# Performance work log

Measured on AMD Instinct MI355X. Metric: run time of the kernel, lower is better.

## Reference

```python
import jax, jax.numpy as jnp
import numpy as np

B, S, D, H = 4, 2048, 1024, 16
DK = D // H


def setup_inputs() -> dict:
    key = jax.random.key(0)
    ks = jax.random.split(key, 5)
    scale = 1.0 / np.sqrt(D)
    return {
        "embeddings": jax.random.normal(ks[0], (B, S, D), dtype=jnp.float32),
        "W_q": jax.random.normal(ks[1], (D, D), dtype=jnp.float32) * scale,
        "W_k": jax.random.normal(ks[2], (D, D), dtype=jnp.float32) * scale,
        "W_v": jax.random.normal(ks[3], (D, D), dtype=jnp.float32) * scale,
        "W_o": jax.random.normal(ks[4], (D, D), dtype=jnp.float32) * scale,
    }


def reference(embeddings, W_q, W_k, W_v, W_o):
    # torch Linear: y = x @ W.T  (weights stored [out, in])
    def proj(x, W):
        # [B,S,D] -> [B,H,S,DK]
        y = jnp.einsum("bsd,ed->bse", x, W)
        return y.reshape(B, S, H, DK).transpose(0, 2, 1, 3)

    Q = proj(embeddings, W_q)
    K = proj(embeddings, W_k)
    V = proj(embeddings, W_v)

    scores = jnp.einsum("bhqd,bhkd->bhqk", Q, K) / jnp.sqrt(jnp.float32(DK))
    p_attn = jax.nn.softmax(scores, axis=-1)  # dropout p=0.0 -> identity
    x = jnp.einsum("bhqk,bhkd->bhqd", p_attn, V)
    x = x.transpose(0, 2, 1, 3).reshape(B, S, D)
    return jnp.einsum("bsd,ed->bse", x, W_o)
```

## Files before the change

### kernel.cpp

```cpp
#include <hip/hip_runtime.h>
#include <hip/hip_bf16.h>

#define BB 4
#define SS 2048
#define DD 1024
#define HH 16
#define MM (BB * SS)

typedef __attribute__((ext_vector_type(8))) short bf16x8;
typedef __attribute__((ext_vector_type(4))) float f32x4;

__device__ __forceinline__ unsigned short f2bf(float f) {
  union { float f; unsigned u; } v; v.f = f;
  unsigned r = v.u + 0x7fffu + ((v.u >> 16) & 1u);
  return (unsigned short)(r >> 16);
}

__device__ __forceinline__ void gl2lds16(const void* g, void* l) {
  __builtin_amdgcn_global_load_lds(
      (const __attribute__((address_space(1))) unsigned int*)g,
      (__attribute__((address_space(3))) unsigned int*)l, 16, 0, 0);
}

__global__ __launch_bounds__(256)
void convall(const float* __restrict__ X, const float* __restrict__ a,
             const float* __restrict__ b, const float* __restrict__ c,
             const float* __restrict__ d, unsigned short* __restrict__ wall,
             unsigned short* __restrict__ xb) {
  int y = blockIdx.y;
  const float* s; unsigned short* o;
  if (y < 4) {
    const float* srcs[4] = {a, b, c, d};
    s = srcs[y]; o = wall + (size_t)y * 1048576;
  } else {
    s = X + (size_t)(y - 4) * 1048576; o = xb + (size_t)(y - 4) * 1048576;
  }
  int i = (blockIdx.x * 256 + threadIdx.x) * 4;
  float4 v = *(const float4*)(s + i);
  ushort4 h4; h4.x = f2bf(v.x); h4.y = f2bf(v.y); h4.z = f2bf(v.z); h4.w = f2bf(v.w);
  *(ushort4*)(o + i) = h4;
}

template<int OMODE>
__global__ __launch_bounds__(256)
void gemm_k(const unsigned short* __restrict__ A16, const unsigned short* __restrict__ Bp,
            void* __restrict__ C0p, void* __restrict__ C1p, void* __restrict__ C2p) {
  __shared__ unsigned short As[32 * 136];
  __shared__ unsigned short Bs[128 * 32];
  const int m0 = blockIdx.x * 128, n0g = blockIdx.y * 128;
  const int tid = threadIdx.x, lane = tid & 63, wave = tid >> 6;
  const int wm = (wave & 1) * 64, wn = (wave >> 1) * 64;
  const int row_in = lane & 15, quad = lane >> 4;

  f32x4 acc[4][4] = {};

  for (int kb = 0; kb < DD; kb += 32) {
    {
      int r = wave * 32 + (lane >> 2);
      const unsigned short* g = Bp + (size_t)(n0g + r) * DD + kb + (lane & 3) * 8;
      gl2lds16(g, Bs + (wave * 32) * 32);
      gl2lds16(g + (size_t)16 * DD, Bs + (wave * 32 + 16) * 32);
      const unsigned short* ga = A16 + (size_t)(m0 + r) * DD + kb + (lane & 3) * 8;
      gl2lds16(ga, As + (wave * 32) * 32);
      gl2lds16(ga + (size_t)16 * DD, As + (wave * 32 + 16) * 32);
    }
    __syncthreads();
    bf16x8 af[4], bfr[4];
#pragma unroll
    for (int i = 0; i < 4; ++i)
      af[i] = *(const bf16x8*)(As + (wm + i * 16 + row_in) * 32 + quad * 8);
#pragma unroll
    for (int j = 0; j < 4; ++j)
      bfr[j] = *(const bf16x8*)(Bs + (wn + j * 16 + row_in) * 32 + quad * 8);
#pragma unroll
    for (int i = 0; i < 4; ++i)
#pragma unroll
      for (int j = 0; j < 4; ++j)
        acc[i][j] = __builtin_amdgcn_mfma_f32_16x16x32_bf16(af[i], bfr[j], acc[i][j], 0, 0, 0);
    __syncthreads();
  }

  if (OMODE == 1) {
    float* Cout = (float*)C0p;
#pragma unroll
    for (int i = 0; i < 4; ++i)
#pragma unroll
      for (int j = 0; j < 4; ++j)
#pragma unroll
        for (int r = 0; r < 4; ++r)
          Cout[(size_t)(m0 + wm + i * 16 + quad * 4 + r) * DD + n0g + wn + j * 16 + row_in] =
              acc[i][j][r];
  } else {
    const int seg = n0g >> 10;
    if (seg < 2) {
      unsigned short* Cout = (unsigned short*)(seg == 0 ? C0p : C1p);
      const int n0 = n0g & 1023;
#pragma unroll
      for (int i = 0; i < 4; ++i)
#pragma unroll
        for (int j = 0; j < 4; ++j)
#pragma unroll
          for (int r = 0; r < 4; ++r)
            Cout[(size_t)(m0 + wm + i * 16 + quad * 4 + r) * DD + n0 + wn + j * 16 + row_in] =
                f2bf(acc[i][j][r]);
    } else {
      unsigned short* Vt = (unsigned short*)C2p;
      unsigned short* Ts = As;
      const int b = m0 >> 11, m_in_b = m0 & 2047;
      const int nv = n0g - 2048;
#pragma unroll
      for (int cn = 0; cn < 4; ++cn) {
        if ((wave >> 1) == (cn >> 1)) {
#pragma unroll
          for (int i = 0; i < 4; ++i)
#pragma unroll
            for (int jj = 0; jj < 2; ++jj)
#pragma unroll
              for (int r = 0; r < 4; ++r) {
                int j = (cn & 1) * 2 + jj;
                Ts[(jj * 16 + row_in) * 136 + wm + i * 16 + quad * 4 + r] = f2bf(acc[i][j][r]);
              }
        }
        __syncthreads();
#pragma unroll
        for (int it = 0; it < 2; ++it) {
          int cc = tid + it * 256;
          int rowL = cc >> 4, o8 = (cc & 15) * 8;
          int cbase = rowL * 136 + (o8 & 64) + ((o8 & 63) >> 2);
          ushort4 lo, hi;
          lo.x = Ts[cbase];      lo.y = Ts[cbase + 16];
          lo.z = Ts[cbase + 32]; lo.w = Ts[cbase + 48];
          hi.x = Ts[cbase + 1];  hi.y = Ts[cbase + 17];
          hi.z = Ts[cbase + 33]; hi.w = Ts[cbase + 49];
          int n = nv + cn * 32 + rowL;
          int h = n >> 6, dd = n & 63;
          unsigned short* dst = Vt + ((size_t)((b * 16 + h) * 64 + dd)) * SS + m_in_b + o8;
          *(ushort4*)dst = lo;
          *(ushort4*)(dst + 4) = hi;
        }
        __syncthreads();
      }
    }
  }
}

__global__ __launch_bounds__(256, 4)
void attn_kernel(const unsigned short* __restrict__ Q, const unsigned short* __restrict__ K,
                 const unsigned short* __restrict__ Vt_g, unsigned short* __restrict__ AO) {
  __shared__ unsigned short Ks[64 * 72];
  __shared__ unsigned short Vs[64 * 72];
  __shared__ unsigned short Ps[128 * 72];
  const int qt = blockIdx.x, bh = blockIdx.y, b = bh >> 4, h = bh & 15;
  const int tid = threadIdx.x, lane = tid & 63, w = tid >> 6;
  const int row_in = lane & 15, quad = lane >> 4;
  const float Cs = 0.180336880f;
  const float C0 = 17.3123405f;
  const size_t qbase = ((size_t)(b * SS + qt * 128)) * DD + h * 64;

  bf16x8 aq[2][2];
#pragma unroll
  for (int m = 0; m < 2; ++m) {
    const unsigned short* qp = Q + qbase + (size_t)(w * 32 + m * 16 + row_in) * DD;
    aq[m][0] = *(const bf16x8*)(qp + quad * 8);
    aq[m][1] = *(const bf16x8*)(qp + 32 + quad * 8);
  }
  f32x4 oacc[2][4] = {};
  float lrow[2][4] = {};
  const int permr = 2 * (row_in >> 2) + (row_in & 1) + 8 * ((row_in >> 1) & 1);
  const int pw_base = (w * 32) * 72;

  for (int kt = 0; kt < SS / 64; ++kt) {
    __syncthreads();
    const size_t kbase = ((size_t)(b * SS + kt * 64)) * DD + h * 64;
#pragma unroll
    for (int i = 0; i < 2; ++i) {
      int c = tid + i * 256, r = c >> 3, o8 = (c & 7) * 8;
      *(uint4*)(Ks + r * 72 + o8) = *(const uint4*)(K + kbase + (size_t)r * DD + o8);
      *(uint4*)(Vs + r * 72 + o8) =
          *(const uint4*)(Vt_g + ((size_t)(bh * 64 + r)) * SS + kt * 64 + o8);
    }
    __syncthreads();

    f32x4 sacc[2][4] = {};
#pragma unroll
    for (int n = 0; n < 4; ++n) {
      bf16x8 bk0 = *(const bf16x8*)(Ks + (n * 16 + row_in) * 72 + quad * 8);
      bf16x8 bk1 = *(const bf16x8*)(Ks + (n * 16 + row_in) * 72 + 32 + quad * 8);
#pragma unroll
      for (int m = 0; m < 2; ++m) {
        sacc[m][n] = __builtin_amdgcn_mfma_f32_16x16x32_bf16(aq[m][0], bk0, sacc[m][n], 0, 0, 0);
        sacc[m][n] = __builtin_amdgcn_mfma_f32_16x16x32_bf16(aq[m][1], bk1, sacc[m][n], 0, 0, 0);
      }
    }

#pragma unroll
    for (int m = 0; m < 2; ++m)
#pragma unroll
      for (int r = 0; r < 4; ++r) {
        int prow = pw_base + (m * 16 + 2 * quad + (r & 1) + 8 * ((r >> 1) & 1)) * 72;
        union { float f; unsigned u; } p0, p1, p2, p3;
        p0.f = __builtin_amdgcn_exp2f(fmaf(sacc[m][0][r], Cs, -C0));
        p1.f = __builtin_amdgcn_exp2f(fmaf(sacc[m][1][r], Cs, -C0));
        p2.f = __builtin_amdgcn_exp2f(fmaf(sacc[m][2][r], Cs, -C0));
        p3.f = __builtin_amdgcn_exp2f(fmaf(sacc[m][3][r], Cs, -C0));
        lrow[m][r] += (p0.f + p1.f) + (p2.f + p3.f);
        unsigned w01 = __builtin_amdgcn_perm(p1.u + 0x8000u, p0.u + 0x8000u, 0x07060302);
        unsigned w23 = __builtin_amdgcn_perm(p3.u + 0x8000u, p2.u + 0x8000u, 0x07060302);
        *(uint2*)(Ps + prow + row_in * 4) = make_uint2(w01, w23);
      }

#pragma unroll
    for (int c = 0; c < 2; ++c) {
      bf16x8 ap0 = *(const bf16x8*)(Ps + pw_base + (permr) * 72 + c * 32 + quad * 8);
      bf16x8 ap1 = *(const bf16x8*)(Ps + pw_base + (16 + permr) * 72 + c * 32 + quad * 8);
#pragma unroll
      for (int t = 0; t < 4; ++t) {
        bf16x8 bv = *(const bf16x8*)(Vs + (t * 16 + row_in) * 72 + c * 32 + quad * 8);
        oacc[0][t] = __builtin_amdgcn_mfma_f32_16x16x32_bf16(ap0, bv, oacc[0][t], 0, 0, 0);
        oacc[1][t] = __builtin_amdgcn_mfma_f32_16x16x32_bf16(ap1, bv, oacc[1][t], 0, 0, 0);
      }
    }
  }

#pragma unroll
  for (int m = 0; m < 2; ++m)
#pragma unroll
    for (int r = 0; r < 4; ++r) {
#pragma unroll
      for (int s = 1; s < 16; s <<= 1) lrow[m][r] += __shfl_xor(lrow[m][r], s, 64);
      float inv = 1.0f / lrow[m][r];
#pragma unroll
      for (int t = 0; t < 4; ++t)
        AO[qbase + (size_t)(w * 32 + m * 16 + quad * 4 + r) * DD + t * 16 + row_in] =
            f2bf(oacc[m][t][r] * inv);
    }
}

extern "C" void kernel_launch(void* const* d_in, const int* in_sizes, int n_in,
                              void* d_out, int out_size, void* d_ws, size_t ws_size,
                              hipStream_t stream) {
  const float* X  = (const float*)d_in[0];
  const float* Wq = (const float*)d_in[1];
  const float* Wk = (const float*)d_in[2];
  const float* Wv = (const float*)d_in[3];
  const float* Wo = (const float*)d_in[4];

  unsigned short* ws   = (unsigned short*)d_ws;
  unsigned short* Qb   = ws;
  unsigned short* Kb   = Qb + (size_t)MM * DD;
  unsigned short* Vtb  = Kb + (size_t)MM * DD;
  unsigned short* Wall = Vtb + (size_t)MM * DD;
  unsigned short* Xb   = (unsigned short*)d_out;
  float* out = (float*)d_out;

  convall<<<dim3(1024, 12), 256, 0, stream>>>(X, Wq, Wk, Wv, Wo, Wall, Xb);

  gemm_k<3><<<dim3(MM / 128, 24), 256, 0, stream>>>(Xb, Wall, Qb, Kb, Vtb);

  attn_kernel<<<dim3(SS / 128, BB * HH), 256, 0, stream>>>(Qb, Kb, Vtb, Qb);

  gemm_k<1><<<dim3(MM / 128, 8), 256, 0, stream>>>(Qb, Wall + (size_t)3 * 1048576,
                                                   out, nullptr, nullptr);
}
```

Baseline: 277.2 us.

## Prefetch next K/V tile into registers, remap blocks, raise MFMA wave priority

The attention loop now loads the next K and V tile from global memory into registers while the current tile is being computed, so global latency overlaps with the MFMA and softmax work instead of sitting between two barriers. Block indices are remapped so that blocks scheduled together share the same batch-head K/V data, which is meant to improve L2 reuse. s_setprio raises wave priority around the MFMA sections to help interleave waves. The prefetch keeps extra live registers, which may pressure the 4-waves occupancy target.

```diff
diff --git a/kernel.cpp b/kernel.cpp
--- a/kernel.cpp
+++ b/kernel.cpp
@@ -150,7 +150,11 @@
   __shared__ unsigned short Ks[64 * 72];
   __shared__ unsigned short Vs[64 * 72];
   __shared__ unsigned short Ps[128 * 72];
-  const int qt = blockIdx.x, bh = blockIdx.y, b = bh >> 4, h = bh & 15;
+  const int L = (blockIdx.y << 4) + blockIdx.x;
+  const int jj = L >> 3;
+  const int qt = jj & 15;
+  const int bh = (L & 7) + ((jj >> 4) << 3);
+  const int b = bh >> 4, h = bh & 15;
   const int tid = threadIdx.x, lane = tid & 63, w = tid >> 6;
   const int row_in = lane & 15, quad = lane >> 4;
   const float Cs = 0.180336880f;
@@ -169,19 +173,36 @@
   const int permr = 2 * (row_in >> 2) + (row_in & 1) + 8 * ((row_in >> 1) & 1);
   const int pw_base = (w * 32) * 72;
 
+  const int r0 = tid >> 3, o80 = (tid & 7) * 8;
+  const int r1 = (tid + 256) >> 3, o81 = o80;
+  const unsigned short* kp0 = K + ((size_t)(b * SS + r0)) * DD + h * 64 + o80;
+  const unsigned short* kp1 = K + ((size_t)(b * SS + r1)) * DD + h * 64 + o81;
+  const unsigned short* vp0 = Vt_g + ((size_t)(bh * 64 + r0)) * SS + o80;
+  const unsigned short* vp1 = Vt_g + ((size_t)(bh * 64 + r1)) * SS + o81;
+
+  uint4 kr0 = *(const uint4*)kp0;
+  uint4 kr1 = *(const uint4*)kp1;
+  uint4 vr0 = *(const uint4*)vp0;
+  uint4 vr1 = *(const uint4*)vp1;
+
   for (int kt = 0; kt < SS / 64; ++kt) {
     __syncthreads();
-    const size_t kbase = ((size_t)(b * SS + kt * 64)) * DD + h * 64;
-#pragma unroll
-    for (int i = 0; i < 2; ++i) {
-      int c = tid + i * 256, r = c >> 3, o8 = (c & 7) * 8;
-      *(uint4*)(Ks + r * 72 + o8) = *(const uint4*)(K + kbase + (size_t)r * DD + o8);
-      *(uint4*)(Vs + r * 72 + o8) =
-          *(const uint4*)(Vt_g + ((size_t)(bh * 64 + r)) * SS + kt * 64 + o8);
-    }
-    __syncthreads();
+    *(uint4*)(Ks + r0 * 72 + o80) = kr0;
+    *(uint4*)(Ks + r1 * 72 + o81) = kr1;
+    *(uint4*)(Vs + r0 * 72 + o80) = vr0;
+    *(uint4*)(Vs + r1 * 72 + o81) = vr1;
+    __syncthreads();
+    if (kt + 1 < SS / 64) {
+      const size_t ko = (size_t)(kt + 1) * 64 * DD;
+      const size_t vo = (size_t)(kt + 1) * 64;
+      kr0 = *(const uint4*)(kp0 + ko);
+      kr1 = *(const uint4*)(kp1 + ko);
+      vr0 = *(const uint4*)(vp0 + vo);
+      vr1 = *(const uint4*)(vp1 + vo);
+    }
 
     f32x4 sacc[2][4] = {};
+    __builtin_amdgcn_s_setprio(1);
 #pragma unroll
     for (int n = 0; n < 4; ++n) {
       bf16x8 bk0 = *(const bf16x8*)(Ks + (n * 16 + row_in) * 72 + quad * 8);
@@ -192,6 +213,7 @@
         sacc[m][n] = __builtin_amdgcn_mfma_f32_16x16x32_bf16(aq[m][1], bk1, sacc[m][n], 0, 0, 0);
       }
     }
+    __builtin_amdgcn_s_setprio(0);
 
 #pragma unroll
     for (int m = 0; m < 2; ++m)
@@ -209,6 +231,7 @@
         *(uint2*)(Ps + prow + row_in * 4) = make_uint2(w01, w23);
       }
 
+    __builtin_amdgcn_s_setprio(1);
 #pragma unroll
     for (int c = 0; c < 2; ++c) {
       bf16x8 ap0 = *(const bf16x8*)(Ps + pw_base + (permr) * 72 + c * 32 + quad * 8);
@@ -220,6 +243,7 @@
         oacc[1][t] = __builtin_amdgcn_mfma_f32_16x16x32_bf16(ap1, bv, oacc[1][t], 0, 0, 0);
       }
     }
+    __builtin_amdgcn_s_setprio(0);
   }
 
 #pragma unroll
```

Result: faster. 269.1 us (-2.9%).
